# Performance work log

Measured on AMD Instinct MI355X. Metric: run time of the kernel, lower is better.

## Reference

```python
import jax, jax.numpy as jnp
import numpy as np
from jax import lax

N, C, F, W = 4096, 1, 15, 120
STRIDE = 10
NW = W // STRIDE            # 12 windows
P = F * (F - 1) // 2        # 105 pairs
HP = 2 * P + 4 * F          # 270 stacked stat rows
FC1_IN = 16 * HP * (NW - 2) # 43200
FC2, FC3, FCAST = 512, 128, 1
BN_EPS = 1e-5

# static pair indices, same order as generate(list(range(F)))
_II, _JJ = np.triu_indices(F, k=1)


def _fill(x):
    # numpy_fill: replace nan/inf with 0
    return jnp.where(jnp.isfinite(x), x, jnp.zeros_like(x))


def setup_inputs() -> dict:
    key = jax.random.key(0)
    ks = jax.random.split(key, 13)
    inp = {
        'data': jax.random.uniform(ks[0], (N, C, F, W), dtype=jnp.float32),
        'bn_gamma': jax.random.normal(ks[1], (C,), dtype=jnp.float32),
        'bn_beta': jax.random.normal(ks[2], (C,), dtype=jnp.float32),
        'bn_mean': jax.random.normal(ks[3], (C,), dtype=jnp.float32) * 0.1,
        'bn_var': jax.random.uniform(ks[4], (C,), dtype=jnp.float32) + 0.5,
        'conv_w': jax.random.normal(ks[5], (16, 1, 1, 3), dtype=jnp.float32) * 0.1,
        'conv_b': jax.random.normal(ks[6], (16,), dtype=jnp.float32) * 0.1,
        'fc1_w': jax.random.normal(ks[7], (FC2, FC1_IN), dtype=jnp.float32) * (1.0 / np.sqrt(FC1_IN)),
        'fc1_b': jax.random.normal(ks[8], (FC2,), dtype=jnp.float32) * 0.01,
        'fc2_w': jax.random.normal(ks[9], (FC3, FC2), dtype=jnp.float32) * (1.0 / np.sqrt(FC2)),
        'fc2_b': jax.random.normal(ks[10], (FC3,), dtype=jnp.float32) * 0.01,
        'fc3_w': jax.random.normal(ks[11], (FCAST, FC3), dtype=jnp.float32) * (1.0 / np.sqrt(FC3)),
        'fc3_b': jax.random.normal(ks[12], (FCAST,), dtype=jnp.float32) * 0.01,
    }
    return inp


def _features(data):
    # data: [N,C,F,W] -> windows [N,C,F,NW,S]
    S = STRIDE
    win = data.reshape(data.shape[0], data.shape[1], F, NW, S)
    mean = win.mean(axis=-1)                         # [N,C,F,NW]
    spread = win - mean[..., None]
    var_u = (spread * spread).sum(axis=-1) / (S - 1)  # unbiased, matches torch .std()
    std = jnp.sqrt(var_u)
    # pairwise cov / corr over (II, JJ)
    cov = (spread[:, :, _II] * spread[:, :, _JJ]).sum(axis=-1) / (S - 1)  # [N,C,P,NW]
    corr = _fill(cov / (std[:, :, _II] * std[:, :, _JJ]) * ((S - 1) / S))
    cov = _fill(cov)
    stdf = _fill(std)
    zs = _fill(mean / std)
    ret = _fill(win[..., -1] / win[..., 0] - 1.0)
    w = jnp.arange(1, S + 1, dtype=jnp.float32)
    w = w / w.sum()
    dl = _fill((win * w).sum(axis=-1))
    # concat along feature rows, order as in forward: corr,cov,std,zscore,return,decaylinear
    return jnp.concatenate([corr, cov, stdf, zs, ret, dl], axis=2)  # [N,C,HP,NW]


def reference(data, bn_gamma, bn_beta, bn_mean, bn_var, conv_w, conv_b,
              fc1_w, fc1_b, fc2_w, fc2_b, fc3_w, fc3_b):
    feat = _features(data)  # [N,1,HP,NW]
    # BatchNorm2d (eval mode, running stats)
    x = (feat - bn_mean[None, :, None, None]) * lax.rsqrt(bn_var + BN_EPS)[None, :, None, None]
    x = x * bn_gamma[None, :, None, None] + bn_beta[None, :, None, None]
    # Conv2d(1,16,(1,3)) valid padding
    x = lax.conv_general_dilated(x, conv_w, window_strides=(1, 1), padding='VALID',
                                 dimension_numbers=('NCHW', 'OIHW', 'NCHW'))
    x = jax.nn.relu(x + conv_b[None, :, None, None])  # [N,16,HP,NW-2]
    x = x.reshape(x.shape[0], -1)                      # [N, FC1_IN]
    # MLP head (dropout = identity in eval)
    x = jax.nn.relu(x @ fc1_w.T + fc1_b)
    x = jax.nn.sigmoid(x @ fc2_w.T + fc2_b)
    out = (x @ fc3_w.T + fc3_b)[:, 0]                  # fc3(...).T[0] -> [N]
    return out
```

## Files before the change

### kernel.cpp

```cpp
#include <hip/hip_runtime.h>
#include <cstdint>
#include <cstddef>


typedef _Float16 f16;
typedef f16 f16x2 __attribute__((ext_vector_type(2)));
typedef f16 f16x8 __attribute__((ext_vector_type(8)));
typedef float f32x4 __attribute__((ext_vector_type(4)));

#define CHUNK   2048
#define K_FC1   43200
#define KT_TOT  675
#define TILE_F  16384
#define HALF_F  8192

__device__ __forceinline__ float fillv(float x) { return isfinite(x) ? x : 0.0f; }

__global__ __launch_bounds__(256) void retile_w(const float* __restrict__ w,
                                                f16* __restrict__ Wt) {
    const int bid = blockIdx.x;
    const int nt = bid / KT_TOT, kt = bid % KT_TOT;
    const int t = threadIdx.x;
    f16* dst = Wt + (size_t)bid * TILE_F;
    #pragma unroll
    for (int j = 0; j < 8; ++j) {
        int q = t + 256 * j;
        int half = q >> 10, rr = (q >> 3) & 127, c = q & 7;
        const float* s = w + (size_t)(nt * 256 + half * 128 + rr) * K_FC1 + kt * 64 + c * 8;
        float4 x = *(const float4*)s;
        float4 y = *(const float4*)(s + 4);
        f16x8 o = { (f16)x.x, (f16)x.y, (f16)x.z, (f16)x.w,
                    (f16)y.x, (f16)y.y, (f16)y.z, (f16)y.w };
        int p = c ^ (rr & 7);
        *(f16x8*)(dst + (size_t)half * HALF_F + rr * 64 + p * 8) = o;
    }
}

__global__ __launch_bounds__(256) void stage_a(
    const float* __restrict__ data, const float* __restrict__ bn_g,
    const float* __restrict__ bn_b, const float* __restrict__ bn_m,
    const float* __restrict__ bn_v, const float* __restrict__ conv_w,
    const float* __restrict__ conv_b, f16* __restrict__ A16, int n0)
{
    __shared__ __align__(16) float pool[5400];
    __shared__ __align__(16) float feat[270 * 12];
    __shared__ float cwf[48];
    __shared__ float cbf[16];
    __shared__ int   pi[105], pj[105];

    float* raw = pool;
    f16*   cstage = (f16*)pool;

    const int t = threadIdx.x;
    const int n = n0 + blockIdx.x;
    const float4* src4 = (const float4*)(data + (size_t)n * 1800);
    for (int i = t; i < 450; i += 256) ((float4*)pool)[i] = src4[i];

    {
        float a  = bn_g[0] * rsqrtf(bn_v[0] + 1e-5f);
        float bb = bn_b[0] - bn_m[0] * a;
        if (t < 48) cwf[t] = conv_w[t] * a;
        if (t < 16) cbf[t] = conv_b[t] + bb * (conv_w[3 * t] + conv_w[3 * t + 1] + conv_w[3 * t + 2]);
    }
    if (t < 105) {
        int i = 0, rem = t;
        while (rem >= 14 - i) { rem -= 14 - i; ++i; }
        pi[t] = i; pj[t] = i + 1 + rem;
    }
    __syncthreads();

    if (t < 180) {
        int f = t / 12, w = t % 12;
        int base = f * 120 + w * 10;
        const float2* r2 = (const float2*)(raw + base);
        float2 p0 = r2[0], p1 = r2[1], p2 = r2[2], p3 = r2[3], p4 = r2[4];
        float x[10] = { p0.x, p0.y, p1.x, p1.y, p2.x, p2.y, p3.x, p3.y, p4.x, p4.y };
        float sum = 0.f;
        #pragma unroll
        for (int s = 0; s < 10; ++s) sum += x[s];
        float mean = sum * 0.1f;
        float ret = x[9] / x[0] - 1.0f;
        float dl = 0.f;
        #pragma unroll
        for (int s = 0; s < 10; ++s) dl += x[s] * ((float)(s + 1) * (1.0f / 55.0f));
        float var = 0.f;
        float d[10];
        #pragma unroll
        for (int s = 0; s < 10; ++s) { d[s] = x[s] - mean; var += d[s] * d[s]; }
        float2* w2p = (float2*)(raw + base);
        #pragma unroll
        for (int s = 0; s < 5; ++s) w2p[s] = make_float2(d[2 * s], d[2 * s + 1]);
        var *= (1.0f / 9.0f);
        float sd = sqrtf(var);
        feat[(210 + f) * 12 + w] = fillv(sd);
        feat[(225 + f) * 12 + w] = fillv(mean / sd);
        feat[(240 + f) * 12 + w] = fillv(ret);
        feat[(255 + f) * 12 + w] = fillv(dl);
    }
    __syncthreads();

    for (int q = t; q < 1260; q += 256) {
        int p = q / 12, w = q % 12;
        int i = pi[p], j = pj[p];
        const float2* ri = (const float2*)(raw + i * 120 + w * 10);
        const float2* rj = (const float2*)(raw + j * 120 + w * 10);
        float cv = 0.f;
        #pragma unroll
        for (int s = 0; s < 5; ++s) {
            float2 ai = ri[s], aj = rj[s];
            cv += ai.x * aj.x + ai.y * aj.y;
        }
        cv *= (1.0f / 9.0f);
        float si = feat[(210 + i) * 12 + w], sj = feat[(210 + j) * 12 + w];
        feat[p * 12 + w]         = fillv(cv / (si * sj) * 0.9f);
        feat[(105 + p) * 12 + w] = fillv(cv);
    }
    __syncthreads();

    const int s_idx = blockIdx.x;
    const int mt = s_idx >> 8, r256 = s_idx & 255;
    const int half = r256 >> 7, rloc = r256 & 127, rsw = r256 & 7;
    f16* abase = A16 + ((size_t)(mt * KT_TOT) * 2 + half) * HALF_F + (size_t)rloc * 64;

    for (int p = 0; p < 4; ++p) {
        #pragma unroll
        for (int j = 0; j < 5; ++j) {
            int item = t + (j << 8);
            if (item < 1080) {
                int h = item >> 2, ocl = item & 3, oc = (p << 2) + ocl;
                const float4* f4 = (const float4*)(feat + h * 12);
                float4 fa = f4[0], fb = f4[1], fc = f4[2];
                float fv[12] = { fa.x, fa.y, fa.z, fa.w,
                                 fb.x, fb.y, fb.z, fb.w,
                                 fc.x, fc.y, fc.z, fc.w };
                float w0 = cwf[oc * 3], w1 = cwf[oc * 3 + 1], w2 = cwf[oc * 3 + 2];
                float bz = cbf[oc];
                int kl = ocl * 2700 + h * 10;
                #pragma unroll
                for (int q = 0; q < 5; ++q) {
                    float y0 = fmaf(w2, fv[2 * q + 2], fmaf(w1, fv[2 * q + 1], fmaf(w0, fv[2 * q], bz)));
                    float y1 = fmaf(w2, fv[2 * q + 3], fmaf(w1, fv[2 * q + 2], fmaf(w0, fv[2 * q + 1], bz)));
                    y0 = fminf(fmaxf(y0, 0.f) * 0.00390625f, 65000.f);
                    y1 = fminf(fmaxf(y1, 0.f) * 0.00390625f, 65000.f);
                    *(f16x2*)(cstage + kl + 2 * q) = f16x2{ (f16)y0, (f16)y1 };
                }
            }
        }
        __syncthreads();
        #pragma unroll
        for (int j = 0; j < 6; ++j) {
            int u = t + (j << 8);
            if (u < 1350) {
                int U = p * 1350 + u;
                int kt = U >> 3, c = U & 7;
                f16x8 ov = *(const f16x8*)(cstage + u * 8);
                *(f16x8*)(abase + (size_t)kt * TILE_F + ((c ^ rsw) << 3)) = ov;
            }
        }
        __syncthreads();
    }
}

__global__ __launch_bounds__(512, 2) void gemm_fc1(const f16* __restrict__ A,
                                                   const f16* __restrict__ W,
                                                   float* __restrict__ Ysum)
{
    extern __shared__ f16 lds[];

    const int bid = blockIdx.x;
    const int mt = bid & 7;
    const int slot = bid >> 3;
    const int nt = slot & 1;
    const int sk = slot >> 1;
    const int kt0 = sk * 42 + (sk < 3 ? sk : 3);
    const int cnt = 42 + (sk < 3 ? 1 : 0);

    const int tid = threadIdx.x;
    const int wave = tid >> 6, lane = tid & 63;
    const int quad = lane >> 4, m16 = lane & 15;
    const int rsw = m16 & 7;
    const int wm = (wave & 1) << 6;
    const int wn = (wave >> 1) << 5;

    const f16* Ab = A + (size_t)(mt * KT_TOT + kt0) * TILE_F;
    const f16* Bb = W + (size_t)(nt * KT_TOT + kt0) * TILE_F;

    f32x4 acc[8][4] = {};
    f16x8 a[4][2], bA[2][2], bB[2][2];

#define STAGE_A(BUF, HALF, KI) do {                                            \
    const f16* g_ = Ab + (size_t)(KI) * TILE_F + (HALF) * HALF_F + tid * 8;    \
    f16* l_ = lds + (BUF) * TILE_F + (HALF) * HALF_F + tid * 8;                \
    __builtin_amdgcn_global_load_lds(                                          \
        (const __attribute__((address_space(1))) void*)g_,                     \
        (__attribute__((address_space(3))) void*)l_, 16, 0, 0);                \
    __builtin_amdgcn_global_load_lds(                                          \
        (const __attribute__((address_space(1))) void*)(g_ + 4096),            \
        (__attribute__((address_space(3))) void*)(l_ + 4096), 16, 0, 0);       \
} while (0)

#define STAGE_B(BUF, HALF, KI) do {                                            \
    const f16* g_ = Bb + (size_t)(KI) * TILE_F + (HALF) * HALF_F + tid * 8;    \
    f16* l_ = lds + 32768 + (BUF) * TILE_F + (HALF) * HALF_F + tid * 8;        \
    __builtin_amdgcn_global_load_lds(                                          \
        (const __attribute__((address_space(1))) void*)g_,                     \
        (__attribute__((address_space(3))) void*)l_, 16, 0, 0);                \
    __builtin_amdgcn_global_load_lds(                                          \
        (const __attribute__((address_space(1))) void*)(g_ + 4096),            \
        (__attribute__((address_space(3))) void*)(l_ + 4096), 16, 0, 0);       \
} while (0)

#define RD_A(MH, BUF) do {                                                     \
    _Pragma("unroll") for (int i2_ = 0; i2_ < 4; ++i2_)                        \
    _Pragma("unroll") for (int kh_ = 0; kh_ < 2; ++kh_)                        \
        a[i2_][kh_] = *(const f16x8*)(lds + (BUF) * TILE_F + (MH) * HALF_F     \
            + (wm + i2_ * 16 + m16) * 64 + (((kh_ * 4 + quad) ^ rsw) << 3));   \
} while (0)

#define RD_B(DST, NH, BUF) do {                                                \
    _Pragma("unroll") for (int j2_ = 0; j2_ < 2; ++j2_)                        \
    _Pragma("unroll") for (int kh_ = 0; kh_ < 2; ++kh_)                        \
        DST[j2_][kh_] = *(const f16x8*)(lds + 32768 + (BUF) * TILE_F           \
            + (NH) * HALF_F                                                    \
            + (wn + j2_ * 16 + m16) * 64 + (((kh_ * 4 + quad) ^ rsw) << 3));   \
} while (0)

#define MMA(IO, JO, BF) do {                                                   \
    _Pragma("unroll") for (int i2_ = 0; i2_ < 4; ++i2_)                        \
    _Pragma("unroll") for (int j2_ = 0; j2_ < 2; ++j2_)                        \
    _Pragma("unroll") for (int kh_ = 0; kh_ < 2; ++kh_)                        \
        acc[(IO) + i2_][(JO) + j2_] = __builtin_amdgcn_mfma_f32_16x16x32_f16(  \
            a[i2_][kh_], BF[j2_][kh_], acc[(IO) + i2_][(JO) + j2_], 0, 0, 0);  \
} while (0)

    STAGE_A(0, 0, 0);
    STAGE_B(0, 0, 0);
    STAGE_B(0, 1, 0);
    STAGE_A(0, 1, 0);
    asm volatile("s_waitcnt vmcnt(4)" ::: "memory");
    __builtin_amdgcn_s_barrier();

    #pragma unroll 1
    for (int ti = 0; ti < cnt - 1; ++ti) {
        const int bc = ti & 1, bn = bc ^ 1;
        RD_A(0, bc); RD_B(bA, 0, bc);
        STAGE_A(bn, 0, ti + 1);
        __builtin_amdgcn_s_barrier();
        __builtin_amdgcn_s_setprio(1);
        MMA(0, 0, bA);
        __builtin_amdgcn_s_setprio(0);
        asm volatile("s_waitcnt vmcnt(4)" ::: "memory");
        __builtin_amdgcn_s_barrier();
        RD_B(bB, 1, bc);
        STAGE_B(bn, 0, ti + 1);
        __builtin_amdgcn_s_barrier();
        __builtin_amdgcn_s_setprio(1);
        MMA(0, 2, bB);
        __builtin_amdgcn_s_setprio(0);
        asm volatile("s_waitcnt vmcnt(4)" ::: "memory");
        __builtin_amdgcn_s_barrier();
        RD_A(1, bc);
        STAGE_B(bn, 1, ti + 1);
        __builtin_amdgcn_s_barrier();
        __builtin_amdgcn_s_setprio(1);
        MMA(4, 2, bB);
        __builtin_amdgcn_s_setprio(0);
        __builtin_amdgcn_s_barrier();
        STAGE_A(bn, 1, ti + 1);
        __builtin_amdgcn_s_barrier();
        __builtin_amdgcn_s_setprio(1);
        MMA(4, 0, bA);
        __builtin_amdgcn_s_setprio(0);
        asm volatile("s_waitcnt vmcnt(4)" ::: "memory");
        __builtin_amdgcn_s_barrier();
    }

    {
        const int bc = (cnt - 1) & 1;
        RD_A(0, bc); RD_B(bA, 0, bc);
        __builtin_amdgcn_s_setprio(1);
        MMA(0, 0, bA);
        __builtin_amdgcn_s_setprio(0);
        asm volatile("s_waitcnt vmcnt(2)" ::: "memory");
        __builtin_amdgcn_s_barrier();
        RD_B(bB, 1, bc);
        __builtin_amdgcn_s_setprio(1);
        MMA(0, 2, bB);
        __builtin_amdgcn_s_setprio(0);
        asm volatile("s_waitcnt vmcnt(0)" ::: "memory");
        __builtin_amdgcn_s_barrier();
        RD_A(1, bc);
        __builtin_amdgcn_s_setprio(1);
        MMA(4, 2, bB);
        MMA(4, 0, bA);
        __builtin_amdgcn_s_setprio(0);
    }

#undef STAGE_A
#undef STAGE_B
#undef RD_A
#undef RD_B
#undef MMA

    float* Yb = Ysum + (size_t)(mt * 256) * 512 + nt * 256;
    #pragma unroll
    for (int i = 0; i < 8; ++i) {
        const int row0 = (i >> 2) * 128 + wm + (i & 3) * 16 + quad * 4;
        #pragma unroll
        for (int j = 0; j < 4; ++j) {
            const int col = (j >> 1) * 128 + wn + (j & 1) * 16 + m16;
            #pragma unroll
            for (int r = 0; r < 4; ++r)
                unsafeAtomicAdd(&Yb[(size_t)(row0 + r) * 512 + col], acc[i][j][r]);
        }
    }
}

__global__ __launch_bounds__(128) void head_fc23(const float* __restrict__ y1s,
                                                 const float* __restrict__ b1,
                                                 const float* __restrict__ w2,
                                                 const float* __restrict__ b2,
                                                 const float* __restrict__ w3,
                                                 const float* __restrict__ b3,
                                                 float* __restrict__ out, int n0)
{
    __shared__ float Ys[8 * 512];
    __shared__ float Y2[8 * 128];
    const int t = threadIdx.x;
    const float4* yb = (const float4*)(y1s + (size_t)blockIdx.x * 8 * 512);
    const float4* b1v = (const float4*)b1;
    for (int i = t; i < 8 * 128; i += 128) {
        float4 s = yb[i];
        float4 bv = b1v[i & 127];
        float4 y;
        y.x = fmaxf(fmaf(s.x, 256.f, bv.x), 0.f);
        y.y = fmaxf(fmaf(s.y, 256.f, bv.y), 0.f);
        y.z = fmaxf(fmaf(s.z, 256.f, bv.z), 0.f);
        y.w = fmaxf(fmaf(s.w, 256.f, bv.w), 0.f);
        ((float4*)Ys)[i] = y;
    }
    __syncthreads();

    float acc[8];
    float bk = b2[t];
    #pragma unroll
    for (int s = 0; s < 8; ++s) acc[s] = bk;
    const float4* wr = (const float4*)(w2 + (size_t)t * 512);
    for (int jc = 0; jc < 128; ++jc) {
        float4 w4 = wr[jc];
        #pragma unroll
        for (int s = 0; s < 8; ++s) {
            float4 y4 = *(const float4*)(Ys + s * 512 + jc * 4);
            acc[s] += w4.x * y4.x + w4.y * y4.y + w4.z * y4.z + w4.w * y4.w;
        }
    }
    #pragma unroll
    for (int s = 0; s < 8; ++s) Y2[s * 128 + t] = 1.0f / (1.0f + expf(-acc[s]));
    __syncthreads();

    if (t < 8) {
        float sm = b3[0];
        #pragma unroll 4
        for (int k = 0; k < 128; ++k) sm += Y2[t * 128 + k] * w3[k];
        out[n0 + blockIdx.x * 8 + t] = sm;
    }
}

extern "C" void kernel_launch(void* const* d_in, const int* in_sizes, int n_in,
                              void* d_out, int out_size, void* d_ws, size_t ws_size,
                              hipStream_t stream)
{
    const float* data = (const float*)d_in[0];
    const float* bn_g = (const float*)d_in[1];
    const float* bn_b = (const float*)d_in[2];
    const float* bn_m = (const float*)d_in[3];
    const float* bn_v = (const float*)d_in[4];
    const float* cw   = (const float*)d_in[5];
    const float* cb   = (const float*)d_in[6];
    const float* fc1w = (const float*)d_in[7];
    const float* fc1b = (const float*)d_in[8];
    const float* fc2w = (const float*)d_in[9];
    const float* fc2b = (const float*)d_in[10];
    const float* fc3w = (const float*)d_in[11];
    const float* fc3b = (const float*)d_in[12];
    float* out = (float*)d_out;

    const size_t A16_BYTES = (size_t)CHUNK * K_FC1 * 2;
    const size_t W16_BYTES = (size_t)512 * K_FC1 * 2;
    const size_t Y1_BYTES  = (size_t)CHUNK * 512 * 4;
    if (ws_size < A16_BYTES + W16_BYTES + Y1_BYTES) return;

    char* ws = (char*)d_ws;
    f16*   A16 = (f16*)ws;
    f16*   W16 = (f16*)(ws + A16_BYTES);
    float* y1s = (float*)(ws + A16_BYTES + W16_BYTES);

    static int smem_set = 0;
    if (!smem_set) {
        hipFuncSetAttribute(reinterpret_cast<const void*>(gemm_fc1),
                            hipFuncAttributeMaxDynamicSharedMemorySize, 131072);
        smem_set = 1;
    }

    retile_w<<<2 * KT_TOT, 256, 0, stream>>>(fc1w, W16);

    for (int c = 0; c < 2; ++c) {
        int n0 = c * CHUNK;
        hipMemsetAsync(y1s, 0, Y1_BYTES, stream);
        stage_a<<<CHUNK, 256, 0, stream>>>(data, bn_g, bn_b, bn_m, bn_v, cw, cb, A16, n0);
        gemm_fc1<<<256, 512, 131072, stream>>>(A16, W16, y1s);
        head_fc23<<<CHUNK / 8, 128, 0, stream>>>(y1s, fc1b, fc2w, fc2b, fc3w, fc3b, out, n0);
    }
}
```

Measured before the change: 545.1 us.

## Simplify FC1 GEMM main loop to one prefetch and one barrier per tile

Replaces the fine-grained interleaved schedule, where each quarter of the next tile's global-to-LDS staging was placed between separate MMA groups with its own waitcnt and barriers, with a simpler double-buffer scheme. All four stages for the next tile are issued at the top of the iteration, the whole tile is computed from the current buffer, then a single vmcnt(0) wait and barrier closes the iteration. The peeled last iteration is folded into the loop with guards. The aim is to cut barrier and synchronisation overhead per k-tile, at the cost of coarser overlap and a full drain of outstanding loads each iteration.

```diff
diff --git a/kernel.cpp b/kernel.cpp
--- a/kernel.cpp
+++ b/kernel.cpp
@@ -237,63 +237,35 @@
     STAGE_B(0, 0, 0);
     STAGE_B(0, 1, 0);
     STAGE_A(0, 1, 0);
-    asm volatile("s_waitcnt vmcnt(4)" ::: "memory");
+    asm volatile("s_waitcnt vmcnt(0)" ::: "memory");
     __builtin_amdgcn_s_barrier();
 
     #pragma unroll 1
-    for (int ti = 0; ti < cnt - 1; ++ti) {
+    for (int ti = 0; ti < cnt; ++ti) {
         const int bc = ti & 1, bn = bc ^ 1;
-        RD_A(0, bc); RD_B(bA, 0, bc);
-        STAGE_A(bn, 0, ti + 1);
-        __builtin_amdgcn_s_barrier();
-        __builtin_amdgcn_s_setprio(1);
-        MMA(0, 0, bA);
-        __builtin_amdgcn_s_setprio(0);
-        asm volatile("s_waitcnt vmcnt(4)" ::: "memory");
-        __builtin_amdgcn_s_barrier();
-        RD_B(bB, 1, bc);
-        STAGE_B(bn, 0, ti + 1);
-        __builtin_amdgcn_s_barrier();
-        __builtin_amdgcn_s_setprio(1);
-        MMA(0, 2, bB);
-        __builtin_amdgcn_s_setprio(0);
-        asm volatile("s_waitcnt vmcnt(4)" ::: "memory");
-        __builtin_amdgcn_s_barrier();
-        RD_A(1, bc);
-        STAGE_B(bn, 1, ti + 1);
-        __builtin_amdgcn_s_barrier();
-        __builtin_amdgcn_s_setprio(1);
-        MMA(4, 2, bB);
-        __builtin_amdgcn_s_setprio(0);
-        __builtin_amdgcn_s_barrier();
-        STAGE_A(bn, 1, ti + 1);
-        __builtin_amdgcn_s_barrier();
-        __builtin_amdgcn_s_setprio(1);
-        MMA(4, 0, bA);
-        __builtin_amdgcn_s_setprio(0);
-        asm volatile("s_waitcnt vmcnt(4)" ::: "memory");
-        __builtin_amdgcn_s_barrier();
-    }
-
-    {
-        const int bc = (cnt - 1) & 1;
+        if (ti + 1 < cnt) {
+            STAGE_A(bn, 0, ti + 1);
+            STAGE_B(bn, 0, ti + 1);
+            STAGE_B(bn, 1, ti + 1);
+            STAGE_A(bn, 1, ti + 1);
+        }
         RD_A(0, bc); RD_B(bA, 0, bc);
         __builtin_amdgcn_s_setprio(1);
         MMA(0, 0, bA);
         __builtin_amdgcn_s_setprio(0);
-        asm volatile("s_waitcnt vmcnt(2)" ::: "memory");
-        __builtin_amdgcn_s_barrier();
         RD_B(bB, 1, bc);
         __builtin_amdgcn_s_setprio(1);
         MMA(0, 2, bB);
         __builtin_amdgcn_s_setprio(0);
-        asm volatile("s_waitcnt vmcnt(0)" ::: "memory");
-        __builtin_amdgcn_s_barrier();
         RD_A(1, bc);
         __builtin_amdgcn_s_setprio(1);
         MMA(4, 2, bB);
         MMA(4, 0, bA);
         __builtin_amdgcn_s_setprio(0);
+        if (ti + 1 < cnt) {
+            asm volatile("s_waitcnt vmcnt(0)" ::: "memory");
+            __builtin_amdgcn_s_barrier();
+        }
     }
 
 #undef STAGE_A
```

New measurement: 550.1 us. Within noise of the previous version (+0.9%).
